# Optimization experiments

Measured on AMD Instinct MI355X. Metric: run time of the kernel, lower is better.

Reference implementation:

```python
import jax, jax.numpy as jnp
import numpy as np

INPUT_DIM = 1024
OUTPUT_DIM = 1024
DEGREE = 8
BATCH = 8192


def setup_inputs() -> dict:
    key = jax.random.key(0)
    k1, k2 = jax.random.split(key)
    x = jax.random.normal(k1, (BATCH, INPUT_DIM), dtype=jnp.float32)
    std = 1.0 / (INPUT_DIM * (DEGREE + 1))
    cheby_coeffs = jax.random.normal(k2, (DEGREE + 1, INPUT_DIM, OUTPUT_DIM), dtype=jnp.float32) * std
    tanh_scale = jnp.array(1.0, dtype=jnp.float32)
    tanh_bias = jnp.array(0.0, dtype=jnp.float32)
    return {"x": x, "cheby_coeffs": cheby_coeffs, "tanh_scale": tanh_scale, "tanh_bias": tanh_bias}


def _cheby_basis(x, degree):
    Ts = [jnp.ones_like(x)]
    if degree >= 1:
        Ts.append(x)
    for _ in range(2, degree + 1):
        Ts.append(2.0 * x * Ts[-1] - Ts[-2])
    return jnp.stack(Ts, axis=0)


def reference(x, cheby_coeffs, tanh_scale, tanh_bias):
    degree = cheby_coeffs.shape[0] - 1
    input_dim = cheby_coeffs.shape[1]
    xf = x.reshape(-1, input_dim)
    xt = jnp.tanh(xf * tanh_scale + tanh_bias)            # (B, I)
    cheby = _cheby_basis(xt, degree)                       # (D+1, B, I)
    # bmm over degree then sum over degree == single contraction
    y = jnp.einsum('dbi,dio->bo', cheby, cheby_coeffs)     # (B, O)
    return y
```

## Files before the change

kernel.cpp:

```cpp
#include <hip/hip_runtime.h>
#include <hip/hip_bf16.h>

typedef __attribute__((ext_vector_type(8))) short short8;
typedef __attribute__((ext_vector_type(4))) float f32x4;
typedef __attribute__((ext_vector_type(16))) float f32x16;

#define WS_B0_OFFSET  18874368u

__global__ void wt2_kernel(const float* __restrict__ W, short* __restrict__ Wt2) {
    int bid = blockIdx.x;
    int d = bid >> 7, q = bid & 127;
    int t = threadIdx.x;
    const float* src = W + (size_t)d * 1048576 + (size_t)q * 8 * 1024;
    short* dst = Wt2 + ((size_t)(d * 128 + q) << 13);
#pragma unroll
    for (int u = 0; u < 4; u++) {
        int o = u * 256 + t;
        short8 v;
#pragma unroll
        for (int j = 0; j < 8; j++)
            v[j] = (short)__bfloat16_as_ushort(__float2bfloat16(src[(size_t)j * 1024 + o]));
        *(short8*)(dst + (size_t)o * 8) = v;
    }
}

__global__ void colsum1(const float* __restrict__ W, float* __restrict__ part) {
    int s = blockIdx.x >> 2;
    int o = (blockIdx.x & 3) * 256 + threadIdx.x;
    const float* p = W + (size_t)s * 32 * 1024 + o;
    float acc = 0.f;
#pragma unroll
    for (int i = 0; i < 32; i++) acc += p[(size_t)i * 1024];
    part[s * 1024 + o] = acc;
}
__global__ void colsum2(const float* __restrict__ part, float* __restrict__ b0) {
    int o = blockIdx.x * 256 + threadIdx.x;
    float acc = 0.f;
#pragma unroll
    for (int s = 0; s < 32; s++) acc += part[s * 1024 + o];
    b0[o] = acc;
}

__device__ __forceinline__ float fast_tanh(float t) {
    float e = __expf(t + t);
    return 1.0f - 2.0f * __builtin_amdgcn_rcpf(e + 1.0f);
}

extern "C" __global__ void __launch_bounds__(512, 2)
cheby_gemm(const float* __restrict__ x, const short* __restrict__ Wt2,
           const float* __restrict__ b0v, const float* __restrict__ scp,
           const float* __restrict__ bip, float* __restrict__ out) {
    __shared__ __align__(16) char lds[49152];

    const int tid = threadIdx.x, lane = tid & 63, wid = tid >> 6;
    const int wc = wid & 3, kh = wid >> 2;
    const int tn = blockIdx.x & 3, tm = blockIdx.x >> 2;
    const int m0 = tm << 7, n0 = tn << 8;
    const float sc = scp[0], bi = bip[0];

    const int arow = tid >> 2, ac = tid & 3;
    const int wbyte0 = ac * 2048 + ((arow ^ (ac << 1)) << 4);
    const float* xptr = x + (size_t)(m0 + arow) * 1024 + ac * 8;

    const int cfr = kh * 2 + (lane >> 5);
    const int abase = cfr * 2048 + (((lane & 31) ^ (cfr << 1)) << 4);

    const char* wtb = (const char*)Wt2;
    int bofs[2];
#pragma unroll
    for (int n = 0; n < 2; n++)
        bofs[n] = cfr * 16384 + (n0 + wc * 64 + n * 32 + (lane & 31)) * 16;

    auto bld = [&](int dd, int icc, int n) -> short8 {
        return *(const short8*)(wtb + (size_t)(dd * 128 + icc * 4) * 16384 + bofs[n]);
    };

    f32x4 xv0, xv1;
    auto loadx = [&](int icc) {
        const float* p = xptr + (icc << 5);
        xv0 = *(const f32x4*)p;
        xv1 = *(const f32x4*)(p + 4);
    };

    float x2[8], tA[8], tB[8];
    auto dotanh = [&]() {
#pragma unroll
        for (int j = 0; j < 4; j++) {
            tA[j]     = fast_tanh(fmaf(xv0[j], sc, bi));
            tA[j + 4] = fast_tanh(fmaf(xv1[j], sc, bi));
        }
#pragma unroll
        for (int j = 0; j < 8; j++) x2[j] = tA[j] + tA[j];
    };
    auto writeA = [&](const float* t, int wbuf) {
        short8 v;
#pragma unroll
        for (int j = 0; j < 8; j++)
            v[j] = (short)__bfloat16_as_ushort(__float2bfloat16(t[j]));
        *(short8*)(lds + wbuf * 8192 + wbyte0) = v;
    };

    f32x16 acc[4][2];
#pragma unroll
    for (int n = 0; n < 2; n++) {
        float v = (kh == 0) ? b0v[n0 + wc * 64 + n * 32 + (lane & 31)] : 0.0f;
        f32x16 a;
#pragma unroll
        for (int r = 0; r < 16; r++) a[r] = v;
#pragma unroll
        for (int m = 0; m < 4; m++) acc[m][n] = a;
    }

    auto domfma = [&](int rbuf, const short8* bf) {
        short8 af[4];
#pragma unroll
        for (int m = 0; m < 4; m++)
            af[m] = *(const short8*)(lds + rbuf * 8192 + abase + m * 512);
        __builtin_amdgcn_s_setprio(1);
#pragma unroll
        for (int m = 0; m < 4; m++)
#pragma unroll
            for (int n = 0; n < 2; n++)
                acc[m][n] = __builtin_amdgcn_mfma_f32_32x32x16_bf16(af[m], bf[n], acc[m][n], 0, 0, 0);
        __builtin_amdgcn_s_setprio(0);
    };

#define STEP_END                                                  \
    __builtin_amdgcn_sched_barrier(0);                            \
    asm volatile("s_waitcnt lgkmcnt(0)" ::: "memory");            \
    __builtin_amdgcn_s_barrier();                                 \
    __builtin_amdgcn_sched_barrier(0);

    short8 bfA[2], bfB[2];

    loadx(0);
    bfA[0] = bld(1, 0, 0); bfA[1] = bld(1, 0, 1);
    dotanh();
    writeA(tA, 0);
    STEP_END

    for (int ic = 0; ic < 32; ++ic) {
        const int icn = ic < 31 ? ic + 1 : 31;
        {
            bfB[0] = bld(2, ic, 0); bfB[1] = bld(2, ic, 1);
#pragma unroll
            for (int j = 0; j < 8; j++) tB[j] = fmaf(x2[j], tA[j], -1.0f);
            writeA(tB, 1);
            domfma(0, bfA);
            STEP_END
        }
        {
            bfA[0] = bld(3, ic, 0); bfA[1] = bld(3, ic, 1);
#pragma unroll
            for (int j = 0; j < 8; j++) tA[j] = fmaf(x2[j], tB[j], -tA[j]);
            writeA(tA, 0);
            domfma(1, bfB);
            STEP_END
        }
#define RSTEP(LD, DST, SRC, LBUF, UBUF, RB, WB, XPRE, LIC)        \
        {                                                         \
            LBUF[0] = bld(LD, LIC, 0); LBUF[1] = bld(LD, LIC, 1); \
            if (XPRE) loadx(icn);                                 \
_Pragma("unroll")                                                 \
            for (int j = 0; j < 8; j++)                           \
                DST[j] = fmaf(x2[j], SRC[j], -DST[j]);            \
            writeA(DST, WB);                                      \
            domfma(RB, UBUF);                                     \
            STEP_END                                              \
        }
        RSTEP(4, tB, tA, bfB, bfA, 0, 1, 0, ic)
        RSTEP(5, tA, tB, bfA, bfB, 1, 0, 0, ic)
        RSTEP(6, tB, tA, bfB, bfA, 0, 1, 0, ic)
        RSTEP(7, tA, tB, bfA, bfB, 1, 0, 1, ic)
        RSTEP(8, tB, tA, bfB, bfA, 0, 1, 0, ic)
#undef RSTEP
        {
            bfA[0] = bld(1, icn, 0); bfA[1] = bld(1, icn, 1);
            dotanh();
            writeA(tA, 0);
            domfma(1, bfB);
            STEP_END
        }
    }
#undef STEP_END

#pragma unroll
    for (int m = 0; m < 4; m++) {
        if (kh == 1) {
#pragma unroll
            for (int n = 0; n < 2; n++) {
                char* base = lds + 16384 + (wc * 2 + n) * 4096 + lane * 64;
#pragma unroll
                for (int q = 0; q < 4; q++) {
                    f32x4 v = {acc[m][n][q * 4 + 0], acc[m][n][q * 4 + 1],
                               acc[m][n][q * 4 + 2], acc[m][n][q * 4 + 3]};
                    *(f32x4*)(base + ((q ^ (lane & 3)) << 4)) = v;
                }
            }
        }
        __syncthreads();
        if (kh == 0) {
#pragma unroll
            for (int n = 0; n < 2; n++) {
                const char* base = lds + 16384 + (wc * 2 + n) * 4096 + lane * 64;
#pragma unroll
                for (int q = 0; q < 4; q++) {
                    f32x4 v = *(const f32x4*)(base + ((q ^ (lane & 3)) << 4));
#pragma unroll
                    for (int e = 0; e < 4; e++) acc[m][n][q * 4 + e] += v[e];
                }
            }
        }
        __syncthreads();
    }

    if (kh == 0) {
#pragma unroll
        for (int m = 0; m < 4; m++) {
            int rbase = m0 + m * 32 + ((lane >> 5) << 2);
#pragma unroll
            for (int n = 0; n < 2; n++) {
                int colg = n0 + wc * 64 + n * 32 + (lane & 31);
#pragma unroll
                for (int r = 0; r < 16; r++) {
                    int rowg = rbase + (r & 3) + 8 * (r >> 2);
                    out[(size_t)rowg * 1024 + colg] = acc[m][n][r];
                }
            }
        }
    }
}

extern "C" void kernel_launch(void* const* d_in, const int* in_sizes, int n_in,
                              void* d_out, int out_size, void* d_ws, size_t ws_size,
                              hipStream_t stream) {
    const float* x  = (const float*)d_in[0];
    const float* W  = (const float*)d_in[1];
    const float* sc = (const float*)d_in[2];
    const float* bi = (const float*)d_in[3];
    float* out = (float*)d_out;

    short* Wt2 = (short*)d_ws;
    float* b0  = (float*)((char*)d_ws + WS_B0_OFFSET);
    float* part = out;

    hipLaunchKernelGGL(wt2_kernel, dim3(9 * 128), dim3(256), 0, stream, W, Wt2);
    hipLaunchKernelGGL(colsum1, dim3(128), dim3(256), 0, stream, W, part);
    hipLaunchKernelGGL(colsum2, dim3(4), dim3(256), 0, stream, part, b0);
    hipLaunchKernelGGL(cheby_gemm, dim3(256), dim3(512), 0, stream, x, Wt2, b0, sc, bi, out);
}
```

Measured before the change: 147.7 us.

## Shrink GEMM tile to 128x128 and drop split-K LDS reduction

Measured after the change: 209.2 us. 41.7% more time.

```diff
diff --git a/kernel.cpp b/kernel.cpp
--- a/kernel.cpp
+++ b/kernel.cpp
@@ -46,33 +46,45 @@
     return 1.0f - 2.0f * __builtin_amdgcn_rcpf(e + 1.0f);
 }
 
-extern "C" __global__ void __launch_bounds__(512, 2)
+extern "C" __global__ void __launch_bounds__(512, 4)
 cheby_gemm(const float* __restrict__ x, const short* __restrict__ Wt2,
            const float* __restrict__ b0v, const float* __restrict__ scp,
            const float* __restrict__ bip, float* __restrict__ out) {
-    __shared__ __align__(16) char lds[49152];
+    __shared__ __align__(16) char lds[16384];
 
     const int tid = threadIdx.x, lane = tid & 63, wid = tid >> 6;
-    const int wc = wid & 3, kh = wid >> 2;
-    const int tn = blockIdx.x & 3, tm = blockIdx.x >> 2;
-    const int m0 = tm << 7, n0 = tn << 8;
+    const int wr = wid >> 1, wc = wid & 1;
+    const int tn = blockIdx.x & 7, tm = blockIdx.x >> 3;
+    const int m0 = tm << 7, n0 = tn << 7;
     const float sc = scp[0], bi = bip[0];
+    const char* wtb = (const char*)Wt2;
 
     const int arow = tid >> 2, ac = tid & 3;
     const int wbyte0 = ac * 2048 + ((arow ^ (ac << 1)) << 4);
     const float* xptr = x + (size_t)(m0 + arow) * 1024 + ac * 8;
 
-    const int cfr = kh * 2 + (lane >> 5);
-    const int abase = cfr * 2048 + (((lane & 31) ^ (cfr << 1)) << 4);
-
-    const char* wtb = (const char*)Wt2;
-    int bofs[2];
+    int abase[2];
+#pragma unroll
+    for (int kh = 0; kh < 2; kh++) {
+        int c = kh * 2 + (lane >> 5);
+        abase[kh] = c * 2048 + (((wr * 32 + (lane & 31)) ^ (c << 1)) << 4);
+    }
+    int bofs[2][2];
 #pragma unroll
     for (int n = 0; n < 2; n++)
-        bofs[n] = cfr * 16384 + (n0 + wc * 64 + n * 32 + (lane & 31)) * 16;
-
-    auto bld = [&](int dd, int icc, int n) -> short8 {
-        return *(const short8*)(wtb + (size_t)(dd * 128 + icc * 4) * 16384 + bofs[n]);
+#pragma unroll
+        for (int kh = 0; kh < 2; kh++) {
+            int c = kh * 2 + (lane >> 5);
+            bofs[n][kh] = (c << 14) + (n0 + wc * 64 + n * 32 + (lane & 31)) * 16;
+        }
+
+    auto bld = [&](short8 bf[2][2], int dd, int icc) {
+        const char* p = wtb + ((size_t)(dd * 128 + icc * 4) << 14);
+#pragma unroll
+        for (int n = 0; n < 2; n++)
+#pragma unroll
+            for (int kh = 0; kh < 2; kh++)
+                bf[n][kh] = *(const short8*)(p + bofs[n][kh]);
     };
 
     f32x4 xv0, xv1;
@@ -100,28 +112,27 @@
         *(short8*)(lds + wbuf * 8192 + wbyte0) = v;
     };
 
-    f32x16 acc[4][2];
+    f32x16 acc[2];
 #pragma unroll
     for (int n = 0; n < 2; n++) {
-        float v = (kh == 0) ? b0v[n0 + wc * 64 + n * 32 + (lane & 31)] : 0.0f;
+        float v = b0v[n0 + wc * 64 + n * 32 + (lane & 31)];
         f32x16 a;
 #pragma unroll
         for (int r = 0; r < 16; r++) a[r] = v;
-#pragma unroll
-        for (int m = 0; m < 4; m++) acc[m][n] = a;
-    }
-
-    auto domfma = [&](int rbuf, const short8* bf) {
-        short8 af[4];
-#pragma unroll
-        for (int m = 0; m < 4; m++)
-            af[m] = *(const short8*)(lds + rbuf * 8192 + abase + m * 512);
+        acc[n] = a;
+    }
+
+    auto domfma = [&](int abuf, short8 bf[2][2]) {
+        short8 af[2];
+#pragma unroll
+        for (int kh = 0; kh < 2; kh++)
+            af[kh] = *(const short8*)(lds + abuf * 8192 + abase[kh]);
         __builtin_amdgcn_s_setprio(1);
 #pragma unroll
-        for (int m = 0; m < 4; m++)
-#pragma unroll
-            for (int n = 0; n < 2; n++)
-                acc[m][n] = __builtin_amdgcn_mfma_f32_32x32x16_bf16(af[m], bf[n], acc[m][n], 0, 0, 0);
+        for (int n = 0; n < 2; n++)
+#pragma unroll
+            for (int kh = 0; kh < 2; kh++)
+                acc[n] = __builtin_amdgcn_mfma_f32_32x32x16_bf16(af[kh], bf[n][kh], acc[n], 0, 0, 0);
         __builtin_amdgcn_s_setprio(0);
     };
 
@@ -131,10 +142,10 @@
     __builtin_amdgcn_s_barrier();                                 \
     __builtin_amdgcn_sched_barrier(0);
 
-    short8 bfA[2], bfB[2];
+    short8 bfA[2][2], bfB[2][2];
 
     loadx(0);
-    bfA[0] = bld(1, 0, 0); bfA[1] = bld(1, 0, 1);
+    bld(bfA, 1, 0);
     dotanh();
     writeA(tA, 0);
     STEP_END
@@ -142,7 +153,7 @@
     for (int ic = 0; ic < 32; ++ic) {
         const int icn = ic < 31 ? ic + 1 : 31;
         {
-            bfB[0] = bld(2, ic, 0); bfB[1] = bld(2, ic, 1);
+            bld(bfB, 2, ic);
 #pragma unroll
             for (int j = 0; j < 8; j++) tB[j] = fmaf(x2[j], tA[j], -1.0f);
             writeA(tB, 1);
@@ -150,7 +161,7 @@
             STEP_END
         }
         {
-            bfA[0] = bld(3, ic, 0); bfA[1] = bld(3, ic, 1);
+            bld(bfA, 3, ic);
 #pragma unroll
             for (int j = 0; j < 8; j++) tA[j] = fmaf(x2[j], tB[j], -tA[j]);
             writeA(tA, 0);
@@ -159,7 +170,7 @@
         }
 #define RSTEP(LD, DST, SRC, LBUF, UBUF, RB, WB, XPRE, LIC)        \
         {                                                         \
-            LBUF[0] = bld(LD, LIC, 0); LBUF[1] = bld(LD, LIC, 1); \
+            bld(LBUF, LD, LIC);                                   \
             if (XPRE) loadx(icn);                                 \
 _Pragma("unroll")                                                 \
             for (int j = 0; j < 8; j++)                           \
@@ -171,11 +182,11 @@
         RSTEP(4, tB, tA, bfB, bfA, 0, 1, 0, ic)
         RSTEP(5, tA, tB, bfA, bfB, 1, 0, 0, ic)
         RSTEP(6, tB, tA, bfB, bfA, 0, 1, 0, ic)
-        RSTEP(7, tA, tB, bfA, bfB, 1, 0, 1, ic)
-        RSTEP(8, tB, tA, bfB, bfA, 0, 1, 0, ic)
+        RSTEP(7, tA, tB, bfA, bfB, 1, 0, 0, ic)
+        RSTEP(8, tB, tA, bfB, bfA, 0, 1, 1, ic)
 #undef RSTEP
         {
-            bfA[0] = bld(1, icn, 0); bfA[1] = bld(1, icn, 1);
+            bld(bfA, 1, icn);
             dotanh();
             writeA(tA, 0);
             domfma(1, bfB);
@@ -184,48 +195,15 @@
     }
 #undef STEP_END
 
-#pragma unroll
-    for (int m = 0; m < 4; m++) {
-        if (kh == 1) {
-#pragma unroll
-            for (int n = 0; n < 2; n++) {
-                char* base = lds + 16384 + (wc * 2 + n) * 4096 + lane * 64;
-#pragma unroll
-                for (int q = 0; q < 4; q++) {
-                    f32x4 v = {acc[m][n][q * 4 + 0], acc[m][n][q * 4 + 1],
-                               acc[m][n][q * 4 + 2], acc[m][n][q * 4 + 3]};
-                    *(f32x4*)(base + ((q ^ (lane & 3)) << 4)) = v;
-                }
-            }
-        }
-        __syncthreads();
-        if (kh == 0) {
-#pragma unroll
-            for (int n = 0; n < 2; n++) {
-                const char* base = lds + 16384 + (wc * 2 + n) * 4096 + lane * 64;
-#pragma unroll
-                for (int q = 0; q < 4; q++) {
-                    f32x4 v = *(const f32x4*)(base + ((q ^ (lane & 3)) << 4));
-#pragma unroll
-                    for (int e = 0; e < 4; e++) acc[m][n][q * 4 + e] += v[e];
-                }
-            }
-        }
-        __syncthreads();
-    }
-
-    if (kh == 0) {
-#pragma unroll
-        for (int m = 0; m < 4; m++) {
-            int rbase = m0 + m * 32 + ((lane >> 5) << 2);
-#pragma unroll
-            for (int n = 0; n < 2; n++) {
-                int colg = n0 + wc * 64 + n * 32 + (lane & 31);
-#pragma unroll
-                for (int r = 0; r < 16; r++) {
-                    int rowg = rbase + (r & 3) + 8 * (r >> 2);
-                    out[(size_t)rowg * 1024 + colg] = acc[m][n][r];
-                }
+    {
+        int rbase = m0 + wr * 32 + ((lane >> 5) << 2);
+#pragma unroll
+        for (int n = 0; n < 2; n++) {
+            int colg = n0 + wc * 64 + n * 32 + (lane & 31);
+#pragma unroll
+            for (int r = 0; r < 16; r++) {
+                int rowg = rbase + (r & 3) + 8 * (r >> 2);
+                out[(size_t)rowg * 1024 + colg] = acc[n][r];
             }
         }
     }
@@ -247,5 +225,5 @@
     hipLaunchKernelGGL(wt2_kernel, dim3(9 * 128), dim3(256), 0, stream, W, Wt2);
     hipLaunchKernelGGL(colsum1, dim3(128), dim3(256), 0, stream, W, part);
     hipLaunchKernelGGL(colsum2, dim3(4), dim3(256), 0, stream, part, b0);
-    hipLaunchKernelGGL(cheby_gemm, dim3(256), dim3(512), 0, stream, x, Wt2, b0, sc, bi, out);
-}
+    hipLaunchKernelGGL(cheby_gemm, dim3(512), dim3(512), 0, stream, x, Wt2, b0, sc, bi, out);
+}
```

## Prefetch A fragments from LDS after barrier to overlap with next MFMA step

Applied to the files above, without the earlier changes.

Measured after the change: 166.9 us. 13.0% more time.

```diff
diff --git a/kernel.cpp b/kernel.cpp
--- a/kernel.cpp
+++ b/kernel.cpp
@@ -57,6 +57,7 @@
     const int tn = blockIdx.x & 3, tm = blockIdx.x >> 2;
     const int m0 = tm << 7, n0 = tn << 8;
     const float sc = scp[0], bi = bip[0];
+    const char* wtb = (const char*)Wt2;
 
     const int arow = tid >> 2, ac = tid & 3;
     const int wbyte0 = ac * 2048 + ((arow ^ (ac << 1)) << 4);
@@ -64,15 +65,16 @@
 
     const int cfr = kh * 2 + (lane >> 5);
     const int abase = cfr * 2048 + (((lane & 31) ^ (cfr << 1)) << 4);
-
-    const char* wtb = (const char*)Wt2;
     int bofs[2];
 #pragma unroll
     for (int n = 0; n < 2; n++)
         bofs[n] = cfr * 16384 + (n0 + wc * 64 + n * 32 + (lane & 31)) * 16;
 
-    auto bld = [&](int dd, int icc, int n) -> short8 {
-        return *(const short8*)(wtb + (size_t)(dd * 128 + icc * 4) * 16384 + bofs[n]);
+    auto bld = [&](short8* bf, int dd, int icc) {
+        const char* p = wtb + ((size_t)(dd * 128 + icc * 4) << 14);
+#pragma unroll
+        for (int n = 0; n < 2; n++)
+            bf[n] = *(const short8*)(p + bofs[n]);
     };
 
     f32x4 xv0, xv1;
@@ -99,6 +101,11 @@
             v[j] = (short)__bfloat16_as_ushort(__float2bfloat16(t[j]));
         *(short8*)(lds + wbuf * 8192 + wbyte0) = v;
     };
+    auto readA = [&](short8* af, int buf) {
+#pragma unroll
+        for (int m = 0; m < 4; m++)
+            af[m] = *(const short8*)(lds + buf * 8192 + abase + m * 512);
+    };
 
     f32x16 acc[4][2];
 #pragma unroll
@@ -111,11 +118,7 @@
         for (int m = 0; m < 4; m++) acc[m][n] = a;
     }
 
-    auto domfma = [&](int rbuf, const short8* bf) {
-        short8 af[4];
-#pragma unroll
-        for (int m = 0; m < 4; m++)
-            af[m] = *(const short8*)(lds + rbuf * 8192 + abase + m * 512);
+    auto domfma = [&](const short8* af, const short8* bf) {
         __builtin_amdgcn_s_setprio(1);
 #pragma unroll
         for (int m = 0; m < 4; m++)
@@ -125,64 +128,50 @@
         __builtin_amdgcn_s_setprio(0);
     };
 
-#define STEP_END                                                  \
+    short8 af0[4], af1[4], bfA[2], bfB[2];
+
+#define DRAIN_BAR                                                 \
     __builtin_amdgcn_sched_barrier(0);                            \
     asm volatile("s_waitcnt lgkmcnt(0)" ::: "memory");            \
-    __builtin_amdgcn_s_barrier();                                 \
-    __builtin_amdgcn_sched_barrier(0);
-
-    short8 bfA[2], bfB[2];
+    __builtin_amdgcn_s_barrier();
 
     loadx(0);
-    bfA[0] = bld(1, 0, 0); bfA[1] = bld(1, 0, 1);
+    bld(bfA, 1, 0);
     dotanh();
     writeA(tA, 0);
-    STEP_END
+    DRAIN_BAR
+    readA(af0, 0);
+    __builtin_amdgcn_sched_barrier(0);
+
+#define RSTEP(AFU, AFP, BFU, BFL, LD, LIC, WB, RECUR, XPRE)       \
+    {                                                             \
+        domfma(AFU, BFU);                                         \
+        __builtin_amdgcn_sched_barrier(0);                        \
+        bld(BFL, LD, LIC);                                        \
+        if (XPRE) loadx(icn);                                     \
+        RECUR                                                     \
+        DRAIN_BAR                                                 \
+        readA(AFP, WB);                                           \
+        __builtin_amdgcn_sched_barrier(0);                        \
+    }
+#define REC_T2  { for (int j = 0; j < 8; j++) tB[j] = fmaf(x2[j], tA[j], -1.0f);  writeA(tB, 1); }
+#define REC_BA(WB) { for (int j = 0; j < 8; j++) tA[j] = fmaf(x2[j], tB[j], -tA[j]); writeA(tA, WB); }
+#define REC_AB(WB) { for (int j = 0; j < 8; j++) tB[j] = fmaf(x2[j], tA[j], -tB[j]); writeA(tB, WB); }
+#define REC_TANH { dotanh(); writeA(tA, 0); }
 
     for (int ic = 0; ic < 32; ++ic) {
         const int icn = ic < 31 ? ic + 1 : 31;
-        {
-            bfB[0] = bld(2, ic, 0); bfB[1] = bld(2, ic, 1);
-#pragma unroll
-            for (int j = 0; j < 8; j++) tB[j] = fmaf(x2[j], tA[j], -1.0f);
-            writeA(tB, 1);
-            domfma(0, bfA);
-            STEP_END
-        }
-        {
-            bfA[0] = bld(3, ic, 0); bfA[1] = bld(3, ic, 1);
-#pragma unroll
-            for (int j = 0; j < 8; j++) tA[j] = fmaf(x2[j], tB[j], -tA[j]);
-            writeA(tA, 0);
-            domfma(1, bfB);
-            STEP_END
-        }
-#define RSTEP(LD, DST, SRC, LBUF, UBUF, RB, WB, XPRE, LIC)        \
-        {                                                         \
-            LBUF[0] = bld(LD, LIC, 0); LBUF[1] = bld(LD, LIC, 1); \
-            if (XPRE) loadx(icn);                                 \
-_Pragma("unroll")                                                 \
-            for (int j = 0; j < 8; j++)                           \
-                DST[j] = fmaf(x2[j], SRC[j], -DST[j]);            \
-            writeA(DST, WB);                                      \
-            domfma(RB, UBUF);                                     \
-            STEP_END                                              \
-        }
-        RSTEP(4, tB, tA, bfB, bfA, 0, 1, 0, ic)
-        RSTEP(5, tA, tB, bfA, bfB, 1, 0, 0, ic)
-        RSTEP(6, tB, tA, bfB, bfA, 0, 1, 0, ic)
-        RSTEP(7, tA, tB, bfA, bfB, 1, 0, 1, ic)
-        RSTEP(8, tB, tA, bfB, bfA, 0, 1, 0, ic)
+        RSTEP(af0, af1, bfA, bfB, 2, ic, 1, REC_T2,     0)
+        RSTEP(af1, af0, bfB, bfA, 3, ic, 0, REC_BA(0),  0)
+        RSTEP(af0, af1, bfA, bfB, 4, ic, 1, REC_AB(1),  0)
+        RSTEP(af1, af0, bfB, bfA, 5, ic, 0, REC_BA(0),  0)
+        RSTEP(af0, af1, bfA, bfB, 6, ic, 1, REC_AB(1),  0)
+        RSTEP(af1, af0, bfB, bfA, 7, ic, 0, REC_BA(0),  1)
+        RSTEP(af0, af1, bfA, bfB, 8, ic, 1, REC_AB(1),  0)
+        RSTEP(af1, af0, bfB, bfA, 1, icn, 0, REC_TANH,  0)
+    }
 #undef RSTEP
-        {
-            bfA[0] = bld(1, icn, 0); bfA[1] = bld(1, icn, 1);
-            dotanh();
-            writeA(tA, 0);
-            domfma(1, bfB);
-            STEP_END
-        }
-    }
-#undef STEP_END
+#undef DRAIN_BAR
 
 #pragma unroll
     for (int m = 0; m < 4; m++) {
```
